# Performance work log

Measured on AMD Instinct MI355X. Metric: run time of the kernel, lower is better.

Reference implementation:

```python
import jax, jax.numpy as jnp
import numpy as np

K = 3          # kernel size
PAD = 1        # padding
# deformable conv v2: offset conv (2*K*K ch), modulator conv (K*K ch, 2*sigmoid), main 3x3 conv, ReLU


def _conv2d(x, w, b):
    y = jax.lax.conv_general_dilated(x, w, (1, 1), ((PAD, PAD), (PAD, PAD)),
                                     dimension_numbers=('NCHW', 'OIHW', 'NCHW'))
    return y + b[None, :, None, None]


def _bilinear_gather(x, py, px):
    # x: [B,C,H,W]; py/px: [B,K2,H,W] float sample coords; zero outside image.
    B, C, H, W = x.shape
    y0 = jnp.floor(py)
    x0 = jnp.floor(px)
    wy1 = py - y0
    wx1 = px - x0
    wy0 = 1.0 - wy1
    wx0 = 1.0 - wx1
    xf = x.reshape(B, C, H * W)

    def gather(yi, xi):
        valid = (yi >= 0) & (yi <= H - 1) & (xi >= 0) & (xi <= W - 1)
        yc = jnp.clip(yi, 0, H - 1).astype(jnp.int32)
        xc = jnp.clip(xi, 0, W - 1).astype(jnp.int32)
        idx = (yc * W + xc).reshape(B, -1)                      # [B, K2*H*W]
        v = jax.vmap(lambda xb, ib: xb[:, ib])(xf, idx)         # [B, C, K2*H*W]
        v = v.reshape(B, C, *yi.shape[1:])                      # [B, C, K2, H, W]
        return v * valid[:, None].astype(x.dtype)

    return (gather(y0, x0) * (wy0 * wx0)[:, None]
            + gather(y0, x0 + 1) * (wy0 * wx1)[:, None]
            + gather(y0 + 1, x0) * (wy1 * wx0)[:, None]
            + gather(y0 + 1, x0 + 1) * (wy1 * wx1)[:, None])


def _deform_conv(data, w, b, w_off, b_off, w_mod, b_mod):
    B, Cin, H, W = data.shape
    off = _conv2d(data, w_off, b_off)                           # [B, 2*K2, H, W]
    mask = 2.0 * jax.nn.sigmoid(_conv2d(data, w_mod, b_mod))    # [B, K2, H, W]
    off = off.reshape(B, K * K, 2, H, W)                        # (dy, dx) per tap
    dy, dx = off[:, :, 0], off[:, :, 1]
    ki, kj = jnp.meshgrid(jnp.arange(K), jnp.arange(K), indexing='ij')
    ki = ki.reshape(-1).astype(data.dtype)
    kj = kj.reshape(-1).astype(data.dtype)
    hs = jnp.arange(H, dtype=data.dtype)
    ws = jnp.arange(W, dtype=data.dtype)
    py = hs[None, None, :, None] - PAD + ki[None, :, None, None] + dy
    px = ws[None, None, None, :] - PAD + kj[None, :, None, None] + dx
    sampled = _bilinear_gather(data, py, px)                    # [B, Cin, K2, H, W]
    sampled = sampled * mask[:, None]
    out = jnp.einsum('bckhw,ock->bohw', sampled, w.reshape(w.shape[0], Cin, K * K))
    return out + b[None, :, None, None]


def setup_inputs() -> dict:
    key = jax.random.key(0)
    ks = jax.random.split(key, 7)
    B, Cin, Cout, H, W = 8, 64, 64, 128, 128
    fan = Cin * K * K
    return {
        'data': jax.random.normal(ks[0], (B, Cin, H, W), jnp.float32),
        'w': jax.random.normal(ks[1], (Cout, Cin, K, K), jnp.float32) / np.sqrt(fan),
        'b': jax.random.normal(ks[2], (Cout,), jnp.float32) * 0.01,
        'w_off': jax.random.normal(ks[3], (2 * K * K, Cin, K, K), jnp.float32) * (0.1 / np.sqrt(fan)),
        'b_off': jnp.zeros((2 * K * K,), jnp.float32),
        'w_mod': jax.random.normal(ks[4], (K * K, Cin, K, K), jnp.float32) * (0.1 / np.sqrt(fan)),
        'b_mod': jnp.zeros((K * K,), jnp.float32),
    }


def reference(data, w, b, w_off, b_off, w_mod, b_mod):
    return jax.nn.relu(_deform_conv(data, w, b, w_off, b_off, w_mod, b_mod))
```

## Files before the change

### kernel.cpp

```cpp
#include <hip/hip_runtime.h>
#include <hip/hip_fp16.h>
#include <cstdint>


typedef _Float16 half8 __attribute__((ext_vector_type(8)));
typedef __attribute__((ext_vector_type(4))) float floatx4;

__device__ __forceinline__ unsigned int pack2h(float lo, float hi) {
    __half2 h = __floats2half2_rn(lo, hi);
    union { __half2 h; unsigned int u; } cv; cv.h = h;
    return cv.u;
}
__device__ __forceinline__ unsigned int blend2h(unsigned int a, unsigned int b,
                                                unsigned int c, unsigned int d,
                                                const __half2* w) {
    union { unsigned int u; __half2 h; } A, B, C, D, O;
    A.u = a; B.u = b; C.u = c; D.u = d;
    __half2 s = __hmul2(A.h, w[0]);
    s = __hfma2(B.h, w[1], s);
    s = __hfma2(C.h, w[2], s);
    s = __hfma2(D.h, w[3], s);
    O.h = s;
    return O.u;
}

#define OFF_DATAT 0u
#define OFF_OFFP  16777216u
#define OFF_WM    30932992u
#define OFF_W27   31006720u
#define OFF_B27   31043584u

__global__ __launch_bounds__(256) void prep_k(const float* __restrict__ x,
                                              unsigned short* __restrict__ xt,
                                              const float* __restrict__ w,
                                              const float* __restrict__ w_off,
                                              const float* __restrict__ w_mod,
                                              const float* __restrict__ b_off,
                                              const float* __restrict__ b_mod,
                                              unsigned short* __restrict__ wpackM,
                                              unsigned short* __restrict__ wq,
                                              float* __restrict__ bias27) {
    __shared__ float tile[64][65];
    int blk = blockIdx.x;
    if (blk < 2048) {
        int b    = blk >> 8;
        int pos0 = (blk & 255) << 6;
        int lane = threadIdx.x & 63;
        int g    = threadIdx.x >> 6;
        for (int c = g; c < 64; c += 4)
            tile[c][lane] = x[(((b << 6) + c) << 14) + pos0 + lane];
        __syncthreads();
        int c2 = lane & 31;
        for (int i = g; i < 32; i += 4) {
            int pr = (i << 1) + (lane >> 5);
            unsigned int d = pack2h(tile[c2 << 1][pr], tile[(c2 << 1) + 1][pr]);
            *(unsigned int*)&xt[((size_t)((b << 14) + pos0 + pr) << 6) + (c2 << 1)] = d;
        }
        return;
    }
    int t = (blk - 2048) * 256 + threadIdx.x;
    if (t < 64 * 576) {
        int o = t / 576, kk = t % 576;
        int k = kk >> 6, c = kk & 63;
        wpackM[t] = __half_as_ushort(__float2half_rn(w[(o * 64 + c) * 9 + k]));
        return;
    }
    t -= 64 * 576;
    if (t < 32 * 576) {
        int o = t / 576, kk = t % 576;
        int k = kk >> 6, c = kk & 63;
        float v = 0.f;
        if (o < 18)      v = w_off[(o * 64 + c) * 9 + k];
        else if (o < 27) v = w_mod[((o - 18) * 64 + c) * 9 + k];
        int s = o >> 4, r = o & 15;
        int chh = c >> 5, q = (c >> 3) & 3, j = c & 7;
        int dst = (((((k << 1) + chh) << 1) + s) << 9) + (q << 7) + (r << 3) + j;
        wq[dst] = __half_as_ushort(__float2half_rn(v));
        if (kk == 0) bias27[o] = (o < 18) ? b_off[o] : (o < 27 ? b_mod[o - 18] : 0.f);
    }
}

__global__ __launch_bounds__(256) void conv27_k(const unsigned short* __restrict__ xt,
                                                const unsigned short* __restrict__ wq,
                                                const float* __restrict__ bias27,
                                                float* __restrict__ offP) {
    int blk   = blockIdx.x;
    int b     = blk >> 7;
    int patch = blk & 127;
    int m     = patch >> 1;
    int h     = patch & 1;
    int tid   = threadIdx.x;
    int lane  = tid & 63, wv = tid >> 6;
    int r = lane & 15, q = lane >> 4;

    const unsigned short* xb = xt + ((size_t)b << 20);
    int rb  = (m << 1) - 1;
    int cxb = (h << 6) + (wv << 4) + r - 1;
    int chq = (q << 3);

    floatx4 acc[4] = {};
    #pragma unroll
    for (int k = 0; k < 9; ++k) {
        int ki = k / 3, kj = k % 3;
        #pragma unroll
        for (int chh = 0; chh < 2; ++chh) {
            int abase = ((((k << 1) + chh) << 1) << 9) + (lane << 3);
            half8 a0 = *(const half8*)&wq[abase];
            half8 a1 = *(const half8*)&wq[abase + 512];
            #pragma unroll
            for (int tr = 0; tr < 2; ++tr) {
                int sy = rb + tr + ki;
                int sx = cxb + kj;
                half8 bf = {};
                if ((unsigned)sy < 128u && (unsigned)sx < 128u)
                    bf = *(const half8*)&xb[(size_t)(((sy << 7) + sx) << 6) + (chh << 5) + chq];
                acc[0 + tr] = __builtin_amdgcn_mfma_f32_16x16x32_f16(a0, bf, acc[0 + tr], 0, 0, 0);
                acc[2 + tr] = __builtin_amdgcn_mfma_f32_16x16x32_f16(a1, bf, acc[2 + tr], 0, 0, 0);
            }
        }
    }

    #pragma unroll
    for (int s = 0; s < 2; ++s) {
        #pragma unroll
        for (int tr = 0; tr < 2; ++tr) {
            #pragma unroll
            for (int reg = 0; reg < 4; ++reg) {
                int oc = (s << 4) + (q << 2) + reg;
                if (oc >= 27) continue;
                int pos = (((m << 1) + tr) << 7) + (h << 6) + (wv << 4) + r;
                float v = acc[(s << 1) + tr][reg] + bias27[oc];
                int kk, comp;
                if (oc < 18) { kk = oc >> 1; comp = oc & 1; }
                else         { kk = oc - 18; comp = 2; v = 2.f / (1.f + __expf(-v)); }
                offP[(size_t)(((b * 9 + kk) * 3 + comp) << 14) + pos] = v;
            }
        }
    }
}

__global__ __launch_bounds__(256, 5) void deform_main_k(const unsigned short* __restrict__ xt,
                                                        const unsigned short* __restrict__ wpackM,
                                                        const float* __restrict__ offP,
                                                        const float* __restrict__ bias,
                                                        float* __restrict__ out) {
    __shared__ ushort4 pOff[576];
    __shared__ uint4   pW[576];
    __shared__ unsigned short samp[2][64][72];
    int blk  = blockIdx.x;
    int b    = blk >> 8;
    int pos0 = (blk & 255) << 6;
    int tid  = threadIdx.x;
    int lane = tid & 63, wv = tid >> 6;
    int r = lane & 15, q = lane >> 4;
    int pg = lane >> 3;
    int j8 = lane & 7;

    const char* xbb = (const char*)(xt + ((size_t)b << 20));

    for (int e = tid; e < 576; e += 256) {
        int k = e >> 6, p = e & 63;
        int pos = pos0 + p;
        const float* offk = offP + ((size_t)((b * 9 + k) * 3) << 14);
        float dy = offk[pos];
        float dx = offk[16384 + pos];
        float m  = offk[32768 + pos];
        float py = (float)(pos >> 7) + (float)(k / 3 - 1) + dy;
        float px = (float)(pos & 127) + (float)(k % 3 - 1) + dx;
        float y0f = floorf(py), x0f = floorf(px);
        int y0 = (int)y0f, x0 = (int)x0f;
        float wy1 = py - y0f, wx1 = px - x0f;
        float wy0 = 1.f - wy1, wx0 = 1.f - wx1;
        bool vy0 = (y0 >= 0) && (y0 < 128);
        bool vy1 = (y0 >= -1) && (y0 < 127);
        bool vx0 = (x0 >= 0) && (x0 < 128);
        bool vx1 = (x0 >= -1) && (x0 < 127);
        float w00 = (vy0 && vx0) ? m * wy0 * wx0 : 0.f;
        float w01 = (vy0 && vx1) ? m * wy0 * wx1 : 0.f;
        float w10 = (vy1 && vx0) ? m * wy1 * wx0 : 0.f;
        float w11 = (vy1 && vx1) ? m * wy1 * wx1 : 0.f;
        int y0c = min(max(y0, 0), 127), y1c = min(max(y0 + 1, 0), 127);
        int x0c = min(max(x0, 0), 127), x1c = min(max(x0 + 1, 0), 127);
        ushort4 io;
        io.x = (unsigned short)((y0c << 7) + x0c);
        io.y = (unsigned short)((y0c << 7) + x1c);
        io.z = (unsigned short)((y1c << 7) + x0c);
        io.w = (unsigned short)((y1c << 7) + x1c);
        pOff[e] = io;
        union { uint4 u; __half2 h[4]; } pw;
        pw.h[0] = __float2half2_rn(w00);
        pw.h[1] = __float2half2_rn(w01);
        pw.h[2] = __float2half2_rn(w10);
        pw.h[3] = __float2half2_rn(w11);
        pW[e] = pw.u;
    }
    __syncthreads();

    floatx4 acc[4] = {};
    const char* xp = xbb + (j8 << 4);
    const unsigned short* wrow = wpackM + ((wv << 4) + r) * 576 + (q << 3);

    uint4   c00[2][2], c01[2][2], c10[2][2], c11[2][2];
    uint4   cwS[2][2];
    ushort4 nio[2];
    uint4   ncw[2];
    half8   afC[2], afN[2];

    auto readParams = [&](int k) {
        #pragma unroll
        for (int i = 0; i < 2; ++i) {
            int e  = (k << 6) + (wv << 4) + (i << 3) + pg;
            nio[i] = pOff[e];
            ncw[i] = pW[e];
        }
    };
    auto issueInto = [&](int s) {
        #pragma unroll
        for (int i = 0; i < 2; ++i) {
            cwS[s][i] = ncw[i];
            c00[s][i] = *(const uint4*)(xp + ((int)nio[i].x << 7));
            c01[s][i] = *(const uint4*)(xp + ((int)nio[i].y << 7));
            c10[s][i] = *(const uint4*)(xp + ((int)nio[i].z << 7));
            c11[s][i] = *(const uint4*)(xp + ((int)nio[i].w << 7));
        }
    };
    auto blendStore = [&](int s, int buf) {
        #pragma unroll
        for (int i = 0; i < 2; ++i) {
            int p = (wv << 4) + (i << 3) + pg;
            union { uint4 u; __half2 h[4]; } W; W.u = cwS[s][i];
            uint4 o4;
            o4.x = blend2h(c00[s][i].x, c01[s][i].x, c10[s][i].x, c11[s][i].x, W.h);
            o4.y = blend2h(c00[s][i].y, c01[s][i].y, c10[s][i].y, c11[s][i].y, W.h);
            o4.z = blend2h(c00[s][i].z, c01[s][i].z, c10[s][i].z, c11[s][i].z, W.h);
            o4.w = blend2h(c00[s][i].w, c01[s][i].w, c10[s][i].w, c11[s][i].w, W.h);
            *(uint4*)&samp[buf][p][j8 << 3] = o4;
        }
    };

    auto ldsBarrier = [&]() {
        asm volatile("s_waitcnt lgkmcnt(0)\n\ts_barrier" ::: "memory");
    };

    readParams(0); issueInto(0);
    readParams(1); issueInto(1);
    afC[0] = *(const half8*)&wrow[0];
    afC[1] = *(const half8*)&wrow[32];
    blendStore(0, 0);
    readParams(2);

    #pragma unroll
    for (int k = 0; k < 9; ++k) {
        if (k <= 6) issueInto(k & 1);
        if (k < 8) {
            afN[0] = *(const half8*)&wrow[((k + 1) << 6)];
            afN[1] = *(const half8*)&wrow[((k + 1) << 6) + 32];
        }
        ldsBarrier();
        #pragma unroll
        for (int ch = 0; ch < 2; ++ch) {
            #pragma unroll
            for (int nt = 0; nt < 4; ++nt) {
                half8 bfrag = *(const half8*)&samp[k & 1][(nt << 4) + r][(ch << 5) + (q << 3)];
                acc[nt] = __builtin_amdgcn_mfma_f32_16x16x32_f16(afC[ch], bfrag, acc[nt], 0, 0, 0);
            }
        }
        if (k < 8) {
            blendStore((k + 1) & 1, (k + 1) & 1);
            if (k <= 5) readParams(k + 3);
            afC[0] = afN[0];
            afC[1] = afN[1];
        }
    }

    #pragma unroll
    for (int nt = 0; nt < 4; ++nt) {
        #pragma unroll
        for (int reg = 0; reg < 4; ++reg) {
            int oc  = (wv << 4) + (q << 2) + reg;
            int pos = pos0 + (nt << 4) + r;
            float v = acc[nt][reg] + bias[oc];
            out[(size_t)(((b << 6) + oc) << 14) + pos] = fmaxf(v, 0.f);
        }
    }
}

extern "C" void kernel_launch(void* const* d_in, const int* in_sizes, int n_in,
                              void* d_out, int out_size, void* d_ws, size_t ws_size,
                              hipStream_t stream) {
    const float* data  = (const float*)d_in[0];
    const float* w     = (const float*)d_in[1];
    const float* bias  = (const float*)d_in[2];
    const float* w_off = (const float*)d_in[3];
    const float* b_off = (const float*)d_in[4];
    const float* w_mod = (const float*)d_in[5];
    const float* b_mod = (const float*)d_in[6];
    float* out = (float*)d_out;

    char* ws = (char*)d_ws;
    unsigned short* dataT   = (unsigned short*)(ws + OFF_DATAT);
    float*          offP    = (float*)(ws + OFF_OFFP);
    unsigned short* wpackM  = (unsigned short*)(ws + OFF_WM);
    unsigned short* wq      = (unsigned short*)(ws + OFF_W27);
    float*          bias27  = (float*)(ws + OFF_B27);

    prep_k<<<2264, 256, 0, stream>>>(data, dataT, w, w_off, w_mod,
                                     b_off, b_mod, wpackM, wq, bias27);
    conv27_k<<<1024, 256, 0, stream>>>(dataT, wq, bias27, offP);
    deform_main_k<<<2048, 256, 0, stream>>>(dataT, wpackM, offP, bias, out);
}
```

Baseline: 196.1 us.

## Keep sampled tile in registers via bpermute, each wave computes all output channels

```diff
diff --git a/kernel.cpp b/kernel.cpp
--- a/kernel.cpp
+++ b/kernel.cpp
@@ -37,7 +37,7 @@
                                               const float* __restrict__ w_mod,
                                               const float* __restrict__ b_off,
                                               const float* __restrict__ b_mod,
-                                              unsigned short* __restrict__ wpackM,
+                                              unsigned short* __restrict__ wqM,
                                               unsigned short* __restrict__ wq,
                                               float* __restrict__ bias27) {
     __shared__ float tile[64][65];
@@ -62,7 +62,10 @@
     if (t < 64 * 576) {
         int o = t / 576, kk = t % 576;
         int k = kk >> 6, c = kk & 63;
-        wpackM[t] = __half_as_ushort(__float2half_rn(w[(o * 64 + c) * 9 + k]));
+        int octile = o >> 4, rr = o & 15;
+        int chh = c >> 5, qq = (c >> 3) & 3, jj = c & 7;
+        int dst = (((k << 3) + (octile << 1) + chh) << 9) + (qq << 7) + (rr << 3) + jj;
+        wqM[dst] = __half_as_ushort(__float2half_rn(w[(o * 64 + c) * 9 + k]));
         return;
     }
     t -= 64 * 576;
@@ -139,14 +142,13 @@
     }
 }
 
-__global__ __launch_bounds__(256, 5) void deform_main_k(const unsigned short* __restrict__ xt,
-                                                        const unsigned short* __restrict__ wpackM,
+__global__ __launch_bounds__(256, 4) void deform_main_k(const unsigned short* __restrict__ xt,
+                                                        const unsigned short* __restrict__ wqM,
                                                         const float* __restrict__ offP,
                                                         const float* __restrict__ bias,
                                                         float* __restrict__ out) {
     __shared__ ushort4 pOff[576];
     __shared__ uint4   pW[576];
-    __shared__ unsigned short samp[2][64][72];
     int blk  = blockIdx.x;
     int b    = blk >> 8;
     int pos0 = (blk & 255) << 6;
@@ -198,13 +200,14 @@
 
     floatx4 acc[4] = {};
     const char* xp = xbb + (j8 << 4);
-    const unsigned short* wrow = wpackM + ((wv << 4) + r) * 576 + (q << 3);
+
+    int idxc0 = ((r & 7) << 5) + (q << 2);
+    int idxc1 = idxc0 + 16;
 
     uint4   c00[2][2], c01[2][2], c10[2][2], c11[2][2];
     uint4   cwS[2][2];
     ushort4 nio[2];
     uint4   ncw[2];
-    half8   afC[2], afN[2];
 
     auto readParams = [&](int k) {
         #pragma unroll
@@ -224,62 +227,61 @@
             c11[s][i] = *(const uint4*)(xp + ((int)nio[i].w << 7));
         }
     };
-    auto blendStore = [&](int s, int buf) {
-        #pragma unroll
-        for (int i = 0; i < 2; ++i) {
-            int p = (wv << 4) + (i << 3) + pg;
-            union { uint4 u; __half2 h[4]; } W; W.u = cwS[s][i];
-            uint4 o4;
-            o4.x = blend2h(c00[s][i].x, c01[s][i].x, c10[s][i].x, c11[s][i].x, W.h);
-            o4.y = blend2h(c00[s][i].y, c01[s][i].y, c10[s][i].y, c11[s][i].y, W.h);
-            o4.z = blend2h(c00[s][i].z, c01[s][i].z, c10[s][i].z, c11[s][i].z, W.h);
-            o4.w = blend2h(c00[s][i].w, c01[s][i].w, c10[s][i].w, c11[s][i].w, W.h);
-            *(uint4*)&samp[buf][p][j8 << 3] = o4;
-        }
+    auto bperm1 = [&](int idx, unsigned int lo, unsigned int hi) -> unsigned int {
+        int t0 = __builtin_amdgcn_ds_bpermute(idx, (int)lo);
+        int t1 = __builtin_amdgcn_ds_bpermute(idx, (int)hi);
+        return (r >= 8) ? (unsigned int)t1 : (unsigned int)t0;
     };
 
-    auto ldsBarrier = [&]() {
-        asm volatile("s_waitcnt lgkmcnt(0)\n\ts_barrier" ::: "memory");
-    };
-
     readParams(0); issueInto(0);
-    readParams(1); issueInto(1);
-    afC[0] = *(const half8*)&wrow[0];
-    afC[1] = *(const half8*)&wrow[32];
-    blendStore(0, 0);
-    readParams(2);
+    readParams(1);
 
     #pragma unroll
     for (int k = 0; k < 9; ++k) {
-        if (k <= 6) issueInto(k & 1);
-        if (k < 8) {
-            afN[0] = *(const half8*)&wrow[((k + 1) << 6)];
-            afN[1] = *(const half8*)&wrow[((k + 1) << 6) + 32];
-        }
-        ldsBarrier();
-        #pragma unroll
-        for (int ch = 0; ch < 2; ++ch) {
+        if (k < 8) issueInto((k + 1) & 1);
+        if (k <= 6) readParams(k + 2);
+
+        uint4 o4[2];
+        {
+            const int s = k & 1;
             #pragma unroll
-            for (int nt = 0; nt < 4; ++nt) {
-                half8 bfrag = *(const half8*)&samp[k & 1][(nt << 4) + r][(ch << 5) + (q << 3)];
-                acc[nt] = __builtin_amdgcn_mfma_f32_16x16x32_f16(afC[ch], bfrag, acc[nt], 0, 0, 0);
+            for (int i = 0; i < 2; ++i) {
+                union { uint4 u; __half2 h[4]; } W; W.u = cwS[s][i];
+                o4[i].x = blend2h(c00[s][i].x, c01[s][i].x, c10[s][i].x, c11[s][i].x, W.h);
+                o4[i].y = blend2h(c00[s][i].y, c01[s][i].y, c10[s][i].y, c11[s][i].y, W.h);
+                o4[i].z = blend2h(c00[s][i].z, c01[s][i].z, c10[s][i].z, c11[s][i].z, W.h);
+                o4[i].w = blend2h(c00[s][i].w, c01[s][i].w, c10[s][i].w, c11[s][i].w, W.h);
             }
         }
-        if (k < 8) {
-            blendStore((k + 1) & 1, (k + 1) & 1);
-            if (k <= 5) readParams(k + 3);
-            afC[0] = afN[0];
-            afC[1] = afN[1];
+
+        uint4 bfu0, bfu1;
+        bfu0.x = bperm1(idxc0, o4[0].x, o4[1].x);
+        bfu0.y = bperm1(idxc0, o4[0].y, o4[1].y);
+        bfu0.z = bperm1(idxc0, o4[0].z, o4[1].z);
+        bfu0.w = bperm1(idxc0, o4[0].w, o4[1].w);
+        bfu1.x = bperm1(idxc1, o4[0].x, o4[1].x);
+        bfu1.y = bperm1(idxc1, o4[0].y, o4[1].y);
+        bfu1.z = bperm1(idxc1, o4[0].z, o4[1].z);
+        bfu1.w = bperm1(idxc1, o4[0].w, o4[1].w);
+        union { uint4 u; half8 h; } B0, B1;
+        B0.u = bfu0; B1.u = bfu1;
+
+        #pragma unroll
+        for (int ot = 0; ot < 4; ++ot) {
+            half8 a0 = *(const half8*)&wqM[(((k << 3) + (ot << 1) + 0) << 9) + (lane << 3)];
+            half8 a1 = *(const half8*)&wqM[(((k << 3) + (ot << 1) + 1) << 9) + (lane << 3)];
+            acc[ot] = __builtin_amdgcn_mfma_f32_16x16x32_f16(a0, B0.h, acc[ot], 0, 0, 0);
+            acc[ot] = __builtin_amdgcn_mfma_f32_16x16x32_f16(a1, B1.h, acc[ot], 0, 0, 0);
         }
     }
 
     #pragma unroll
-    for (int nt = 0; nt < 4; ++nt) {
+    for (int ot = 0; ot < 4; ++ot) {
         #pragma unroll
         for (int reg = 0; reg < 4; ++reg) {
-            int oc  = (wv << 4) + (q << 2) + reg;
-            int pos = pos0 + (nt << 4) + r;
-            float v = acc[nt][reg] + bias[oc];
+            int oc  = (ot << 4) + (q << 2) + reg;
+            int pos = pos0 + (wv << 4) + r;
+            float v = acc[ot][reg] + bias[oc];
             out[(size_t)(((b << 6) + oc) << 14) + pos] = fmaxf(v, 0.f);
         }
     }
@@ -300,12 +302,12 @@
     char* ws = (char*)d_ws;
     unsigned short* dataT   = (unsigned short*)(ws + OFF_DATAT);
     float*          offP    = (float*)(ws + OFF_OFFP);
-    unsigned short* wpackM  = (unsigned short*)(ws + OFF_WM);
+    unsigned short* wqM     = (unsigned short*)(ws + OFF_WM);
     unsigned short* wq      = (unsigned short*)(ws + OFF_W27);
     float*          bias27  = (float*)(ws + OFF_B27);
 
     prep_k<<<2264, 256, 0, stream>>>(data, dataT, w, w_off, w_mod,
-                                     b_off, b_mod, wpackM, wq, bias27);
+                                     b_off, b_mod, wqM, wq, bias27);
     conv27_k<<<1024, 256, 0, stream>>>(dataT, wq, bias27, offP);
-    deform_main_k<<<2048, 256, 0, stream>>>(dataT, wpackM, offP, bias, out);
-}
+    deform_main_k<<<2048, 256, 0, stream>>>(dataT, wqM, offP, bias, out);
+}
```

After: 166.3 us. -15.2%, faster.
